# Performance work log

Hardware: AMD Instinct MI355X
Metric: run time of the kernel (lower is better)

Reference implementation:

```python
import jax, jax.numpy as jnp
import numpy as np

MAX_DISP = 48


def setup_inputs() -> dict:
    key = jax.random.key(0)
    k1, k2 = jax.random.split(key)
    b, c, h, w = 8, 128, 96, 320
    left_feature = jax.random.normal(k1, (b, c, h, w), dtype=jnp.float32)
    right_feature = jax.random.normal(k2, (b, c, h, w), dtype=jnp.float32)
    return {"left_feature": left_feature, "right_feature": right_feature}


def reference(left_feature, right_feature):
    # Correlation cost volume: cost[b, i, h, x] = mean_c left[b,c,h,x] * right[b,c,h,x-i]
    # for x >= i, zero elsewhere. Loop is over the fixed disparity count (48),
    # each iteration touching only the valid width slice (honors the sparsity
    # structure of the original; no [b,c,h,D,w] intermediate is materialized).
    b, c, h, w = left_feature.shape
    slices = []
    for i in range(MAX_DISP):
        if i > 0:
            corr = (left_feature[:, :, :, i:] * right_feature[:, :, :, : w - i]).mean(axis=1)
            corr = jnp.pad(corr, ((0, 0), (0, 0), (i, 0)))  # zeros for x < i
        else:
            corr = (left_feature * right_feature).mean(axis=1)
        slices.append(corr)
    return jnp.stack(slices, axis=1)  # (b, max_disp, h, w)
```

## Files before the change

kernel.cpp:

```cpp
#include <hip/hip_runtime.h>
#include <stdint.h>


typedef __bf16 bf16x8 __attribute__((ext_vector_type(8)));
typedef float floatx16 __attribute__((ext_vector_type(16)));

constexpr int W = 320, H = 96, C = 128, NB = 8, MAXD = 48;
constexpr int HW = H * W;
constexpr int SC = 16;
constexpr int NST = C / SC;
constexpr int TPP = W / 32;
constexpr int NTASK = NB * H * TPP;
constexpr int WPB = 4;
constexpr int ESZ = MAXD * 33;

__device__ __forceinline__ uint32_t pack_bf16x2(float a, float b) {
    uint32_t ua = __float_as_uint(a), ub = __float_as_uint(b);
    uint32_t lo = (ua + 0x7fffu + ((ua >> 16) & 1u)) >> 16;
    uint32_t hi = (ub + 0x7fffu + ((ub >> 16) & 1u)) & 0xffff0000u;
    return hi | lo;
}

__device__ __forceinline__ bf16x8 packf(const float* v) {
    uint4 q;
    q.x = pack_bf16x2(v[0], v[1]);
    q.y = pack_bf16x2(v[2], v[3]);
    q.z = pack_bf16x2(v[4], v[5]);
    q.w = pack_bf16x2(v[6], v[7]);
    return __builtin_bit_cast(bf16x8, q);
}

__global__ __launch_bounds__(256, 3) void cost_volume_kernel(
    const float* __restrict__ Lg, const float* __restrict__ Rg,
    float* __restrict__ out)
{
    __shared__ float scr[WPB * ESZ];

    const int t    = threadIdx.x;
    const int lane = t & 63;
    const int w    = t >> 6;
    const int n    = lane & 31;
    const int half = lane >> 5;

    const int wid   = blockIdx.x * WPB + w;
    const int plane = wid / TPP;
    const int p     = wid % TPP;
    const int b     = plane / H;
    const int h     = plane % H;

    const int baseLR = b * (C * HW) + h * W;
    const int lofs = (8 * half) * HW + p * 32 + n;
    const float* Ap  = Lg + baseLR + lofs;
    const float* Bp0 = Rg + baseLR + lofs;
    const float* Bp1 = Bp0 - 32;
    const float* Bp2 = Bp0 - 64;

    float a_[2][8], b0_[2][8], b1_[2][8], b2_[2][8];

#define LOAD_STAGE(BUF, S)                                                  \
    {                                                                       \
        const int o = (S) * SC * HW;                                        \
        _Pragma("unroll")                                                   \
        for (int j = 0; j < 8; ++j) a_[BUF][j] = Ap[o + j * HW];            \
        _Pragma("unroll")                                                   \
        for (int j = 0; j < 8; ++j) b0_[BUF][j] = Bp0[o + j * HW];          \
        if (p >= 1) {                                                       \
            _Pragma("unroll")                                               \
            for (int j = 0; j < 8; ++j) b1_[BUF][j] = Bp1[o + j * HW];      \
        }                                                                   \
        if (p >= 2) {                                                       \
            _Pragma("unroll")                                               \
            for (int j = 0; j < 8; ++j) b2_[BUF][j] = Bp2[o + j * HW];      \
        }                                                                   \
    }

    floatx16 acc0 = 0.f, acc1 = 0.f, acc2 = 0.f;

    LOAD_STAGE(0, 0)

#pragma unroll
    for (int s = 0; s < NST; ++s) {
        const int cur = s & 1;
        const int nxt = cur ^ 1;
        if (s + 1 < NST) LOAD_STAGE(nxt, s + 1)
        bf16x8 af = packf(a_[cur]);
        acc0 = __builtin_amdgcn_mfma_f32_32x32x16_bf16(
            af, packf(b0_[cur]), acc0, 0, 0, 0);
        if (p >= 1)
            acc1 = __builtin_amdgcn_mfma_f32_32x32x16_bf16(
                af, packf(b1_[cur]), acc1, 0, 0, 0);
        if (p >= 2)
            acc2 = __builtin_amdgcn_mfma_f32_32x32x16_bf16(
                af, packf(b2_[cur]), acc2, 0, 0, 0);
    }
#undef LOAD_STAGE

    float* sS = scr + w * ESZ;
    const int ob = b * (MAXD * HW) + h * W + p * 32;
    constexpr float scale = 1.f / 128.f;

    if (p < 2) {
        for (int e = lane; e < ESZ; e += 64) sS[e] = 0.f;
    }

#define FILL_TILE(DP, ACC)                                                  \
    if (p >= (DP)) {                                                        \
        _Pragma("unroll")                                                   \
        for (int r = 0; r < 16; ++r) {                                      \
            int m = (r & 3) + 8 * (r >> 2) + 4 * half;                      \
            int i = 32 * (DP) + m - n;                                      \
            if (i >= 0 && i < MAXD)                                         \
                sS[i * 33 + m] = ACC[r] * scale;                            \
        }                                                                   \
    }
    FILL_TILE(0, acc0)
    FILL_TILE(1, acc1)
    FILL_TILE(2, acc2)
#undef FILL_TILE

#pragma unroll
    for (int e = 0; e < 24; ++e) {
        int idx = e * 64 + lane;
        int i = idx >> 5;
        int m = idx & 31;
        out[ob + i * HW + m] = sS[i * 33 + m];
    }
}

extern "C" void kernel_launch(void* const* d_in, const int* in_sizes, int n_in,
                              void* d_out, int out_size, void* d_ws, size_t ws_size,
                              hipStream_t stream) {
    const float* L = (const float*)d_in[0];
    const float* R = (const float*)d_in[1];
    float* out = (float*)d_out;
    cost_volume_kernel<<<dim3(NTASK / WPB), dim3(64 * WPB), 0, stream>>>(L, R, out);
}
```

Measured before the change: 275.9 us.

## Stream L/R channel chunks via global_load_lds DMA with one-wave blocks

Replaces per-lane strided scalar global loads into registers with 16-byte global_load_lds transfers into a double-buffered LDS ring, prefetching two channel chunks ahead and waiting on vmcnt. Blocks shrink from four waves to one, and each block gets its own LDS buffer, which is reused as the epilogue scratch. The aim is wider, coalesced global reads, fewer vector registers, and overlap of loads with MFMA work. In exchange it loads the full 96-column R window even for p<2, and one-wave blocks with LDS use may limit occupancy. The reuse of the LDS ring for the epilogue is only separated from in-flight DMA by the vmcnt(0) wait, with no extra barrier.

```diff
diff --git a/kernel.cpp b/kernel.cpp
--- a/kernel.cpp
+++ b/kernel.cpp
@@ -7,11 +7,12 @@
 
 constexpr int W = 320, H = 96, C = 128, NB = 8, MAXD = 48;
 constexpr int HW = H * W;
-constexpr int SC = 16;
-constexpr int NST = C / SC;
+constexpr int CH = 16;
+constexpr int NCH = C / CH;
 constexpr int TPP = W / 32;
 constexpr int NTASK = NB * H * TPP;
-constexpr int WPB = 4;
+constexpr int ABD = CH * 32;
+constexpr int BBD = CH * 96;
 constexpr int ESZ = MAXD * 33;
 
 __device__ __forceinline__ uint32_t pack_bf16x2(float a, float b) {
@@ -30,72 +31,101 @@
     return __builtin_bit_cast(bf16x8, q);
 }
 
-__global__ __launch_bounds__(256, 3) void cost_volume_kernel(
+#define GLDS16(gp, lp)                                                     \
+    __builtin_amdgcn_global_load_lds(                                      \
+        (const __attribute__((address_space(1))) void*)(gp),               \
+        (__attribute__((address_space(3))) void*)(lp), 16, 0, 0)
+
+__global__ __launch_bounds__(64) void cost_volume_kernel(
     const float* __restrict__ Lg, const float* __restrict__ Rg,
     float* __restrict__ out)
 {
-    __shared__ float scr[WPB * ESZ];
+    __shared__ uint32_t lds[2 * ABD + 2 * BBD];
 
-    const int t    = threadIdx.x;
-    const int lane = t & 63;
-    const int w    = t >> 6;
+    const int lane = threadIdx.x & 63;
     const int n    = lane & 31;
     const int half = lane >> 5;
 
-    const int wid   = blockIdx.x * WPB + w;
+    const int wid   = blockIdx.x;
     const int plane = wid / TPP;
     const int p     = wid % TPP;
     const int b     = plane / H;
     const int h     = plane % H;
 
     const int baseLR = b * (C * HW) + h * W;
-    const int lofs = (8 * half) * HW + p * 32 + n;
-    const float* Ap  = Lg + baseLR + lofs;
-    const float* Bp0 = Rg + baseLR + lofs;
-    const float* Bp1 = Bp0 - 32;
-    const float* Bp2 = Bp0 - 64;
+    const int pcl    = (p < 2) ? p : 2;
+    const int s0     = 32 * (p - pcl);
 
-    float a_[2][8], b0_[2][8], b1_[2][8], b2_[2][8];
+    const float* gA = Lg + baseLR + (lane >> 3) * HW + 32 * p + (lane & 7) * 4;
+    const float* gB[6];
+#pragma unroll
+    for (int i = 0; i < 6; ++i) {
+        int Q = i * 64 + lane;
+        gB[i] = Rg + baseLR + (Q / 24) * HW + s0 + (Q % 24) * 4;
+    }
 
-#define LOAD_STAGE(BUF, S)                                                  \
-    {                                                                       \
-        const int o = (S) * SC * HW;                                        \
-        _Pragma("unroll")                                                   \
-        for (int j = 0; j < 8; ++j) a_[BUF][j] = Ap[o + j * HW];            \
-        _Pragma("unroll")                                                   \
-        for (int j = 0; j < 8; ++j) b0_[BUF][j] = Bp0[o + j * HW];          \
-        if (p >= 1) {                                                       \
-            _Pragma("unroll")                                               \
-            for (int j = 0; j < 8; ++j) b1_[BUF][j] = Bp1[o + j * HW];      \
-        }                                                                   \
-        if (p >= 2) {                                                       \
-            _Pragma("unroll")                                               \
-            for (int j = 0; j < 8; ++j) b2_[BUF][j] = Bp2[o + j * HW];      \
-        }                                                                   \
-    }
+    auto dmaChunk = [&](int cc) {
+        const int go = CH * cc * HW;
+        uint32_t* dA = lds + (cc & 1) * ABD;
+        GLDS16(gA + go, dA);
+        GLDS16(gA + go + 8 * HW, dA + 256);
+        uint32_t* dB = lds + 2 * ABD + (cc & 1) * BBD;
+#pragma unroll
+        for (int i = 0; i < 6; ++i) GLDS16(gB[i] + go, dB + i * 256);
+    };
 
     floatx16 acc0 = 0.f, acc1 = 0.f, acc2 = 0.f;
 
-    LOAD_STAGE(0, 0)
+    dmaChunk(0);
+    dmaChunk(1);
 
 #pragma unroll
-    for (int s = 0; s < NST; ++s) {
-        const int cur = s & 1;
-        const int nxt = cur ^ 1;
-        if (s + 1 < NST) LOAD_STAGE(nxt, s + 1)
-        bf16x8 af = packf(a_[cur]);
+    for (int cc = 0; cc < NCH; ++cc) {
+        if (cc + 1 < NCH)
+            asm volatile("s_waitcnt vmcnt(8)" ::: "memory");
+        else
+            asm volatile("s_waitcnt vmcnt(0)" ::: "memory");
+
+        const float* Af = reinterpret_cast<const float*>(lds + (cc & 1) * ABD)
+                        + 8 * half * 32 + n;
+        const float* Bb = reinterpret_cast<const float*>(lds + 2 * ABD + (cc & 1) * BBD)
+                        + 8 * half * 96 + n;
+        float av[8], b0v[8], b1v[8], b2v[8];
+#pragma unroll
+        for (int k = 0; k < 8; ++k) av[k] = Af[k * 32];
+        {
+            const float* Bf = Bb + 32 * pcl;
+#pragma unroll
+            for (int k = 0; k < 8; ++k) b0v[k] = Bf[k * 96];
+        }
+        if (p >= 1) {
+            const float* Bf = Bb + 32 * (pcl - 1);
+#pragma unroll
+            for (int k = 0; k < 8; ++k) b1v[k] = Bf[k * 96];
+        }
+        if (p >= 2) {
+            const float* Bf = Bb + 32 * (pcl - 2);
+#pragma unroll
+            for (int k = 0; k < 8; ++k) b2v[k] = Bf[k * 96];
+        }
+
+        asm volatile("s_waitcnt lgkmcnt(0)" ::: "memory");
+        __builtin_amdgcn_sched_barrier(0);
+        if (cc + 2 < NCH) dmaChunk(cc + 2);
+
+        bf16x8 af = packf(av);
         acc0 = __builtin_amdgcn_mfma_f32_32x32x16_bf16(
-            af, packf(b0_[cur]), acc0, 0, 0, 0);
+            af, packf(b0v), acc0, 0, 0, 0);
         if (p >= 1)
             acc1 = __builtin_amdgcn_mfma_f32_32x32x16_bf16(
-                af, packf(b1_[cur]), acc1, 0, 0, 0);
+                af, packf(b1v), acc1, 0, 0, 0);
         if (p >= 2)
             acc2 = __builtin_amdgcn_mfma_f32_32x32x16_bf16(
-                af, packf(b2_[cur]), acc2, 0, 0, 0);
+                af, packf(b2v), acc2, 0, 0, 0);
     }
-#undef LOAD_STAGE
 
-    float* sS = scr + w * ESZ;
+    asm volatile("s_waitcnt lgkmcnt(0)" ::: "memory");
+    float* sS = reinterpret_cast<float*>(lds);
     const int ob = b * (MAXD * HW) + h * W + p * 32;
     constexpr float scale = 1.f / 128.f;
 
@@ -133,5 +163,5 @@
     const float* L = (const float*)d_in[0];
     const float* R = (const float*)d_in[1];
     float* out = (float*)d_out;
-    cost_volume_kernel<<<dim3(NTASK / WPB), dim3(64 * WPB), 0, stream>>>(L, R, out);
+    cost_volume_kernel<<<dim3(NTASK), dim3(64), 0, stream>>>(L, R, out);
 }
```

New measurement: 285.3 us. 1.03x slower.
